# Optimization experiments

Measured on AMD Instinct MI355X. Metric: run time of the kernel, lower is better.

The kernel has to match this reference:

```python
import jax, jax.numpy as jnp
import numpy as np

BETA = 1.0
EPS = 1e-8  # matches torch F.cosine_similarity eps


def setup_inputs() -> dict:
    key = jax.random.key(0)
    x = jax.random.normal(key, (4096, 2, 1024), dtype=jnp.float32)
    return {"x": x}


def _cosine_sim_matrix(pos, anc):
    # pos: [B, D], anc: [B, D] -> [B, B], sim[i, j] = cos(pos[i], anc[j])
    dots = jnp.einsum('id,jd->ij', pos, anc)
    pn = jnp.sqrt(jnp.sum(pos * pos, axis=-1))
    an = jnp.sqrt(jnp.sum(anc * anc, axis=-1))
    denom = jnp.maximum(pn[:, None] * an[None, :], EPS)
    return dots / denom


def reference(x):
    # x: [B, M, D], M >= 2
    out_anchor = jnp.mean(x[:, 1:, :], axis=1)   # [B, D]
    out_positive = x[:, 0, :]                     # [B, D]
    sim = _cosine_sim_matrix(out_positive, out_anchor)  # [B, B]
    n = sim.shape[0]

    diag = jnp.diagonal(sim)                      # [B]
    # tempsim for column i: beta * (sim[:, i] - sim[i, i]), excluding row i
    T = BETA * (sim - diag[None, :])              # [B, B]
    eye = jnp.eye(n, dtype=bool)

    # exclude-diagonal logsumexp per column (vectorized over all columns)
    Tm = jnp.where(eye, -jnp.inf, T)
    temploss = jax.nn.logsumexp(Tm, axis=0)       # [B]
    # flatNCE trick: exp(l - stop_grad(l)) has value 1 but gradient of l
    nloss = jnp.mean(jnp.exp(temploss - jax.lax.stop_gradient(temploss)))

    # top-1 accuracy against labels arange(B) (detached in original)
    label = jnp.arange(n)
    prec1 = jnp.mean((jnp.argmax(sim, axis=1) == label).astype(jnp.float32)) * 100.0
    return nloss, prec1
```

## Files before the change

### kernel.cpp

```cpp
#include <hip/hip_runtime.h>


#define NROWS 4096
#define DDIM  1024
#define XSTR  2048

typedef unsigned int u32;
typedef unsigned long long u64;
typedef __attribute__((ext_vector_type(8))) short bf16x8;
typedef __attribute__((ext_vector_type(8))) unsigned short u16x8;
typedef __attribute__((ext_vector_type(16))) float f32x16;

__device__ __forceinline__ unsigned int fkey(float f) {
    unsigned int u = __float_as_uint(f);
    return (u & 0x80000000u) ? ~u : (u | 0x80000000u);
}

__device__ __forceinline__ u64 shfl_xor_u64(u64 v, int m) {
    unsigned int lo = (unsigned int)v;
    unsigned int hi = (unsigned int)(v >> 32);
    lo = __shfl_xor(lo, m, 64);
    hi = __shfl_xor(hi, m, 64);
    return ((u64)hi << 32) | lo;
}

__device__ __forceinline__ unsigned short f2bf(float f) {
    unsigned u = __float_as_uint(f);
    return (unsigned short)((u + 0x7FFFu + ((u >> 16) & 1u)) >> 16);
}

#define PF_OFF   0u
#define AF_OFF   8388608u
#define INV_OFF  16777216u
#define PCK_OFF  16793600u
#define DONE_OFF 16826368u
#define WS_NEED  16826432u

__global__ __launch_bounds__(256) void norms2_kernel(const float* __restrict__ x,
                                                     float* __restrict__ inv_an,
                                                     u64* __restrict__ packed,
                                                     unsigned int* __restrict__ done) {
    int gid  = blockIdx.x * 256 + threadIdx.x;
    int j    = gid >> 6;
    int lane = threadIdx.x & 63;
    if (gid < NROWS) packed[gid] = 0ULL;
    if (gid == 0) *done = 0u;
    const float4* a = (const float4*)(x + (size_t)j * XSTR + DDIM);
    float s = 0.0f;
#pragma unroll
    for (int i = 0; i < 4; ++i) {
        float4 v = a[lane + i * 64];
        s += v.x * v.x + v.y * v.y + v.z * v.z + v.w * v.w;
    }
#pragma unroll
    for (int off = 32; off > 0; off >>= 1) s += __shfl_down(s, off, 64);
    if (lane == 0) inv_an[j] = 1.0f / sqrtf(s);
}

__global__ __launch_bounds__(256) void conv_kernel(const float* __restrict__ x,
                                                   unsigned short* __restrict__ Pf,
                                                   unsigned short* __restrict__ Af) {
    const int cid  = blockIdx.x * 256 + threadIdx.x;
    const int lane = cid & 63;
    const int kh   = (cid >> 6) & 63;
    const int fb   = cid >> 12;
    const int row  = fb * 32 + (lane & 31);
    const int col  = kh * 16 + (lane >> 5) * 8;

    const float* px = x + (size_t)row * XSTR + col;
    float4 p0 = *(const float4*)(px);
    float4 p1 = *(const float4*)(px + 4);
    float4 a0 = *(const float4*)(px + DDIM);
    float4 a1 = *(const float4*)(px + DDIM + 4);

    u16x8 pv, av;
    pv[0] = f2bf(p0.x); pv[1] = f2bf(p0.y); pv[2] = f2bf(p0.z); pv[3] = f2bf(p0.w);
    pv[4] = f2bf(p1.x); pv[5] = f2bf(p1.y); pv[6] = f2bf(p1.z); pv[7] = f2bf(p1.w);
    av[0] = f2bf(a0.x); av[1] = f2bf(a0.y); av[2] = f2bf(a0.z); av[3] = f2bf(a0.w);
    av[4] = f2bf(a1.x); av[5] = f2bf(a1.y); av[6] = f2bf(a1.z); av[7] = f2bf(a1.w);

    *(u16x8*)(Pf + (size_t)cid * 8) = pv;
    *(u16x8*)(Af + (size_t)cid * 8) = av;
}

__global__ __launch_bounds__(512, 2) void mfma_gemm_argmax(const unsigned short* __restrict__ Pf,
                                                           const unsigned short* __restrict__ Af,
                                                           const float* __restrict__ inv_an,
                                                           u64* __restrict__ packed,
                                                           unsigned int* __restrict__ done,
                                                           float* __restrict__ out) {
    __shared__ __align__(16) unsigned int lds[32768];
    __shared__ unsigned int lastflag;
    __shared__ int cnt[8];

    const int bid = blockIdx.x;
    const int xcd = bid & 7;
    const int slt = bid >> 3;
    const int rblk = (xcd >> 1) * 4 + (slt >> 3);
    const int cblk = (xcd & 1) * 8 + (slt & 7);
    const int r0 = rblk * 256;
    const int c0 = cblk * 256;

    const int wave = threadIdx.x >> 6;
    const int lane = threadIdx.x & 63;
    const int l31 = lane & 31;
    const int lh = lane >> 5;
    const int wm = wave & 3;
    const int wn = wave >> 2;

    const char* gPs = (const char*)Pf + (((size_t)(rblk * 8 + wave)) << 16) + (size_t)lane * 16;
    const char* gAs = (const char*)Af + (((size_t)(cblk * 8 + wave)) << 16) + (size_t)lane * 16;

    f32x16 zero16 = {0.f,0.f,0.f,0.f,0.f,0.f,0.f,0.f,0.f,0.f,0.f,0.f,0.f,0.f,0.f,0.f};
    f32x16 acc[2][4];
#pragma unroll
    for (int i = 0; i < 2; ++i)
#pragma unroll
        for (int j = 0; j < 4; ++j) acc[i][j] = zero16;

#define ISSUE_TILE(tt)                                                                  \
    {                                                                                   \
        const int sb_ = ((tt) & 3) * 8192;                                              \
        const size_t go_ = ((size_t)((tt) * 2)) << 10;                                  \
        __builtin_amdgcn_global_load_lds((const u32*)(gPs + go_),                       \
                                         &lds[sb_ + wave * 256], 16, 0, 0);             \
        __builtin_amdgcn_global_load_lds((const u32*)(gAs + go_),                       \
                                         &lds[sb_ + 4096 + wave * 256], 16, 0, 0);      \
        __builtin_amdgcn_global_load_lds((const u32*)(gPs + go_ + 1024),                \
                                         &lds[sb_ + 2048 + wave * 256], 16, 0, 0);      \
        __builtin_amdgcn_global_load_lds((const u32*)(gAs + go_ + 1024),                \
                                         &lds[sb_ + 4096 + 2048 + wave * 256], 16, 0, 0);\
    }

#define PHASE(kh_l)                                                                     \
    {                                                                                   \
        const u32* bp_ = &lds[cbuf + (kh_l) * 2048 + (wm * 2) * 256 + lane * 4];        \
        bf16x8 f_p0 = *(const bf16x8*)(bp_);                                            \
        bf16x8 f_p1 = *(const bf16x8*)(bp_ + 256);                                      \
        const u32* ba_ = &lds[cbuf + 4096 + (kh_l) * 2048 + (wn * 4) * 256 + lane * 4]; \
        bf16x8 f_a0 = *(const bf16x8*)(ba_);                                            \
        bf16x8 f_a1 = *(const bf16x8*)(ba_ + 256);                                      \
        bf16x8 f_a2 = *(const bf16x8*)(ba_ + 512);                                      \
        bf16x8 f_a3 = *(const bf16x8*)(ba_ + 768);                                      \
        __builtin_amdgcn_s_barrier();                                                   \
        asm volatile("s_waitcnt lgkmcnt(0)" ::: "memory");                              \
        __builtin_amdgcn_sched_barrier(0);                                              \
        __builtin_amdgcn_s_setprio(1);                                                  \
        acc[0][0] = __builtin_amdgcn_mfma_f32_32x32x16_bf16(f_p0, f_a0, acc[0][0], 0, 0, 0); \
        acc[0][1] = __builtin_amdgcn_mfma_f32_32x32x16_bf16(f_p0, f_a1, acc[0][1], 0, 0, 0); \
        acc[0][2] = __builtin_amdgcn_mfma_f32_32x32x16_bf16(f_p0, f_a2, acc[0][2], 0, 0, 0); \
        acc[0][3] = __builtin_amdgcn_mfma_f32_32x32x16_bf16(f_p0, f_a3, acc[0][3], 0, 0, 0); \
        acc[1][0] = __builtin_amdgcn_mfma_f32_32x32x16_bf16(f_p1, f_a0, acc[1][0], 0, 0, 0); \
        acc[1][1] = __builtin_amdgcn_mfma_f32_32x32x16_bf16(f_p1, f_a1, acc[1][1], 0, 0, 0); \
        acc[1][2] = __builtin_amdgcn_mfma_f32_32x32x16_bf16(f_p1, f_a2, acc[1][2], 0, 0, 0); \
        acc[1][3] = __builtin_amdgcn_mfma_f32_32x32x16_bf16(f_p1, f_a3, acc[1][3], 0, 0, 0); \
        __builtin_amdgcn_s_setprio(0);                                                  \
        __builtin_amdgcn_s_barrier();                                                   \
    }

    ISSUE_TILE(0)
    ISSUE_TILE(1)
    ISSUE_TILE(2)

    for (int t = 0; t < 32; ++t) {
        const int cbuf = (t & 3) * 8192;

        if (t + 3 < 32) ISSUE_TILE(t + 3)

        if      (t < 29)  asm volatile("s_waitcnt vmcnt(12)" ::: "memory");
        else if (t == 29) asm volatile("s_waitcnt vmcnt(8)" ::: "memory");
        else if (t == 30) asm volatile("s_waitcnt vmcnt(4)" ::: "memory");
        else              asm volatile("s_waitcnt vmcnt(0)" ::: "memory");
        __builtin_amdgcn_s_barrier();

        PHASE(0)
        PHASE(1)
    }

    float ian[4];
#pragma unroll
    for (int nt = 0; nt < 4; ++nt) ian[nt] = inv_an[c0 + wn * 128 + nt * 32 + l31];

#pragma unroll
    for (int mt = 0; mt < 2; ++mt)
#pragma unroll
        for (int reg = 0; reg < 16; ++reg) {
            const int row = r0 + wm * 64 + mt * 32 + (reg & 3) + 8 * (reg >> 2) + 4 * lh;
            u64 best = 0ULL;
#pragma unroll
            for (int nt = 0; nt < 4; ++nt) {
                const int col = c0 + wn * 128 + nt * 32 + l31;
                const float v = acc[mt][nt][reg] * ian[nt];
                const u64 p = ((u64)fkey(v) << 32) | (unsigned int)(~col);
                best = best > p ? best : p;
            }
#pragma unroll
            for (int m = 1; m <= 16; m <<= 1) {
                const u64 o = shfl_xor_u64(best, m);
                best = best > o ? best : o;
            }
            if (l31 == 0) atomicMax(&packed[row], best);
        }

    __syncthreads();
    if (threadIdx.x == 0) {
        __threadfence();
        unsigned int old = atomicAdd(done, 1u);
        lastflag = (old == 255u) ? 1u : 0u;
    }
    __syncthreads();
    if (lastflag) {
        int c = 0;
        for (int r = threadIdx.x; r < NROWS; r += 512) {
            u64 v = atomicAdd(&packed[r], 0ULL);
            unsigned int col = ~(unsigned int)(v & 0xFFFFFFFFULL);
            c += (col == (unsigned int)r) ? 1 : 0;
        }
#pragma unroll
        for (int off = 32; off > 0; off >>= 1) c += __shfl_down(c, off, 64);
        if ((threadIdx.x & 63) == 0) cnt[threadIdx.x >> 6] = c;
        __syncthreads();
        if (threadIdx.x == 0) {
            int tot = 0;
#pragma unroll
            for (int w = 0; w < 8; ++w) tot += cnt[w];
            out[0] = 1.0f;
            out[1] = 100.0f * (float)tot / (float)NROWS;
        }
    }
#undef ISSUE_TILE
#undef PHASE
}

__global__ __launch_bounds__(256) void norms_kernel(const float* __restrict__ x,
                                                    float* __restrict__ inv_an,
                                                    u64* __restrict__ packed) {
    int gid  = blockIdx.x * 256 + threadIdx.x;
    int j    = gid >> 6;
    int lane = threadIdx.x & 63;
    if (gid < NROWS) packed[gid] = 0ULL;
    const float4* a = (const float4*)(x + (size_t)j * XSTR + DDIM);
    float s = 0.0f;
#pragma unroll
    for (int i = 0; i < 4; ++i) {
        float4 v = a[lane + i * 64];
        s += v.x * v.x + v.y * v.y + v.z * v.z + v.w * v.w;
    }
#pragma unroll
    for (int off = 32; off > 0; off >>= 1) s += __shfl_down(s, off, 64);
    if (lane == 0) inv_an[j] = 1.0f / sqrtf(s);
}

__global__ __launch_bounds__(256) void gemm_argmax_kernel(const float* __restrict__ x,
                                                          const float* __restrict__ inv_an,
                                                          u64* __restrict__ packed) {
    __shared__ __align__(16) float Pt[16][128];
    __shared__ __align__(16) float At[16][128];
    const int r0 = blockIdx.x * 128;
    const int c0 = blockIdx.y * 128;
    const int t = threadIdx.x;
    const int tx = t & 15;
    const int ty = t >> 4;
    const int srow = t >> 1;
    const int skq = (t & 1) * 8;
    float acc[8][8];
#pragma unroll
    for (int r = 0; r < 8; ++r)
#pragma unroll
        for (int c = 0; c < 8; ++c) acc[r][c] = 0.0f;
    const float* gp = x + (size_t)(r0 + srow) * XSTR + skq;
    const float* ga = x + (size_t)(c0 + srow) * XSTR + DDIM + skq;
    for (int k0 = 0; k0 < DDIM; k0 += 16) {
        __syncthreads();
        float4 p0 = *(const float4*)(gp + k0);
        float4 p1 = *(const float4*)(gp + k0 + 4);
        float4 a0 = *(const float4*)(ga + k0);
        float4 a1 = *(const float4*)(ga + k0 + 4);
        Pt[skq + 0][srow] = p0.x; Pt[skq + 1][srow] = p0.y;
        Pt[skq + 2][srow] = p0.z; Pt[skq + 3][srow] = p0.w;
        Pt[skq + 4][srow] = p1.x; Pt[skq + 5][srow] = p1.y;
        Pt[skq + 6][srow] = p1.z; Pt[skq + 7][srow] = p1.w;
        At[skq + 0][srow] = a0.x; At[skq + 1][srow] = a0.y;
        At[skq + 2][srow] = a0.z; At[skq + 3][srow] = a0.w;
        At[skq + 4][srow] = a1.x; At[skq + 5][srow] = a1.y;
        At[skq + 6][srow] = a1.z; At[skq + 7][srow] = a1.w;
        __syncthreads();
#pragma unroll
        for (int kk = 0; kk < 16; ++kk) {
            float pr[8], ar[8];
            *(float4*)&pr[0] = *(const float4*)&Pt[kk][ty * 8];
            *(float4*)&pr[4] = *(const float4*)&Pt[kk][ty * 8 + 4];
            *(float4*)&ar[0] = *(const float4*)&At[kk][tx * 8];
            *(float4*)&ar[4] = *(const float4*)&At[kk][tx * 8 + 4];
#pragma unroll
            for (int r = 0; r < 8; ++r)
#pragma unroll
                for (int c = 0; c < 8; ++c) acc[r][c] += pr[r] * ar[c];
        }
    }
    float ian[8];
#pragma unroll
    for (int c = 0; c < 8; ++c) ian[c] = inv_an[c0 + tx * 8 + c];
#pragma unroll
    for (int r = 0; r < 8; ++r) {
        int row = r0 + ty * 8 + r;
        u64 best = 0ULL;
#pragma unroll
        for (int c = 0; c < 8; ++c) {
            int col = c0 + tx * 8 + c;
            float v = acc[r][c] * ian[c];
            u64 p = ((u64)fkey(v) << 32) | (unsigned int)(~col);
            best = best > p ? best : p;
        }
#pragma unroll
        for (int m = 1; m <= 8; m <<= 1) {
            u64 o = shfl_xor_u64(best, m);
            best = best > o ? best : o;
        }
        if (tx == 0) atomicMax(&packed[row], best);
    }
}

__global__ __launch_bounds__(256) void finalize_kernel(const u64* __restrict__ packed,
                                                       float* __restrict__ out) {
    __shared__ int cnt_s;
    int t = threadIdx.x;
    if (t == 0) cnt_s = 0;
    __syncthreads();
    int c = 0;
    for (int r = t; r < NROWS; r += 256) {
        unsigned int col = ~(unsigned int)(packed[r] & 0xFFFFFFFFULL);
        c += (col == (unsigned int)r) ? 1 : 0;
    }
#pragma unroll
    for (int off = 32; off > 0; off >>= 1) c += __shfl_down(c, off, 64);
    if ((t & 63) == 0) atomicAdd(&cnt_s, c);
    __syncthreads();
    if (t == 0) {
        out[0] = 1.0f;
        out[1] = 100.0f * (float)cnt_s / (float)NROWS;
    }
}

extern "C" void kernel_launch(void* const* d_in, const int* in_sizes, int n_in,
                              void* d_out, int out_size, void* d_ws, size_t ws_size,
                              hipStream_t stream) {
    (void)in_sizes; (void)n_in; (void)out_size;
    const float* x = (const float*)d_in[0];
    float* out = (float*)d_out;

    if (ws_size >= (size_t)WS_NEED) {
        char* ws = (char*)d_ws;
        unsigned short* Pf = (unsigned short*)(ws + PF_OFF);
        unsigned short* Af = (unsigned short*)(ws + AF_OFF);
        float* inv_an = (float*)(ws + INV_OFF);
        u64* packed = (u64*)(ws + PCK_OFF);
        unsigned int* done = (unsigned int*)(ws + DONE_OFF);

        norms2_kernel<<<NROWS / 4, 256, 0, stream>>>(x, inv_an, packed, done);
        conv_kernel<<<2048, 256, 0, stream>>>(x, Pf, Af);
        mfma_gemm_argmax<<<256, 512, 0, stream>>>(Pf, Af, inv_an, packed, done, out);
    } else {
        float* inv_an = (float*)d_ws;
        u64* packed = (u64*)((char*)d_ws + NROWS * sizeof(float));
        norms_kernel<<<NROWS / 4, 256, 0, stream>>>(x, inv_an, packed);
        dim3 grid(NROWS / 128, NROWS / 128);
        gemm_argmax_kernel<<<grid, 256, 0, stream>>>(x, inv_an, packed);
        finalize_kernel<<<1, 256, 0, stream>>>(packed, out);
    }
}
```

Before: 131.2 us.

## Shrink GEMM block tile to 128x256 with 4 waves and double-buffered LDS

The fused GEMM+argmax kernel moves from 512-thread blocks with 256x256 tiles to 256-thread blocks with 128x256 tiles, doubling the grid to 512 blocks. The 4-deep LDS ring with graduated vmcnt waits is replaced by a 2-stage double buffer (48 KB instead of 128 KB) that waits for all loads each iteration, and the per-phase barriers are dropped. The goal is more blocks per CU and less LDS pressure. The cost is more reloading of A tiles and a shallower prefetch that may expose global-load latency.

```diff
diff --git a/kernel.cpp b/kernel.cpp
--- a/kernel.cpp
+++ b/kernel.cpp
@@ -83,33 +83,34 @@
     *(u16x8*)(Af + (size_t)cid * 8) = av;
 }
 
-__global__ __launch_bounds__(512, 2) void mfma_gemm_argmax(const unsigned short* __restrict__ Pf,
+__global__ __launch_bounds__(256, 2) void mfma_gemm_argmax(const unsigned short* __restrict__ Pf,
                                                            const unsigned short* __restrict__ Af,
                                                            const float* __restrict__ inv_an,
                                                            u64* __restrict__ packed,
                                                            unsigned int* __restrict__ done,
                                                            float* __restrict__ out) {
-    __shared__ __align__(16) unsigned int lds[32768];
+    __shared__ __align__(16) unsigned int lds[12288];
     __shared__ unsigned int lastflag;
-    __shared__ int cnt[8];
+    __shared__ int cnt[4];
 
     const int bid = blockIdx.x;
     const int xcd = bid & 7;
     const int slt = bid >> 3;
-    const int rblk = (xcd >> 1) * 4 + (slt >> 3);
+    const int rblk = (xcd >> 1) * 8 + (slt >> 3);
     const int cblk = (xcd & 1) * 8 + (slt & 7);
-    const int r0 = rblk * 256;
+    const int r0 = rblk * 128;
     const int c0 = cblk * 256;
 
     const int wave = threadIdx.x >> 6;
     const int lane = threadIdx.x & 63;
     const int l31 = lane & 31;
     const int lh = lane >> 5;
-    const int wm = wave & 3;
-    const int wn = wave >> 2;
-
-    const char* gPs = (const char*)Pf + (((size_t)(rblk * 8 + wave)) << 16) + (size_t)lane * 16;
-    const char* gAs = (const char*)Af + (((size_t)(cblk * 8 + wave)) << 16) + (size_t)lane * 16;
+    const int wm = wave & 1;
+    const int wn = wave >> 1;
+
+    const char* gPs = (const char*)Pf + (((size_t)(rblk * 4 + wave)) << 16) + (size_t)lane * 16;
+    const char* gA0 = (const char*)Af + (((size_t)(cblk * 8 + wave)) << 16) + (size_t)lane * 16;
+    const char* gA1 = (const char*)Af + (((size_t)(cblk * 8 + wave + 4)) << 16) + (size_t)lane * 16;
 
     f32x16 zero16 = {0.f,0.f,0.f,0.f,0.f,0.f,0.f,0.f,0.f,0.f,0.f,0.f,0.f,0.f,0.f,0.f};
     f32x16 acc[2][4];
@@ -118,34 +119,33 @@
 #pragma unroll
         for (int j = 0; j < 4; ++j) acc[i][j] = zero16;
 
-#define ISSUE_TILE(tt)                                                                  \
+#define ISSUE_TILE(tt, bb)                                                              \
     {                                                                                   \
-        const int sb_ = ((tt) & 3) * 8192;                                              \
         const size_t go_ = ((size_t)((tt) * 2)) << 10;                                  \
         __builtin_amdgcn_global_load_lds((const u32*)(gPs + go_),                       \
-                                         &lds[sb_ + wave * 256], 16, 0, 0);             \
-        __builtin_amdgcn_global_load_lds((const u32*)(gAs + go_),                       \
-                                         &lds[sb_ + 4096 + wave * 256], 16, 0, 0);      \
+                                         &lds[(bb) + wave * 256], 16, 0, 0);            \
         __builtin_amdgcn_global_load_lds((const u32*)(gPs + go_ + 1024),                \
-                                         &lds[sb_ + 2048 + wave * 256], 16, 0, 0);      \
-        __builtin_amdgcn_global_load_lds((const u32*)(gAs + go_ + 1024),                \
-                                         &lds[sb_ + 4096 + 2048 + wave * 256], 16, 0, 0);\
+                                         &lds[(bb) + 1024 + wave * 256], 16, 0, 0);     \
+        __builtin_amdgcn_global_load_lds((const u32*)(gA0 + go_),                       \
+                                         &lds[(bb) + 2048 + wave * 256], 16, 0, 0);     \
+        __builtin_amdgcn_global_load_lds((const u32*)(gA0 + go_ + 1024),                \
+                                         &lds[(bb) + 4096 + wave * 256], 16, 0, 0);     \
+        __builtin_amdgcn_global_load_lds((const u32*)(gA1 + go_),                       \
+                                         &lds[(bb) + 2048 + (wave + 4) * 256], 16, 0, 0);\
+        __builtin_amdgcn_global_load_lds((const u32*)(gA1 + go_ + 1024),                \
+                                         &lds[(bb) + 4096 + (wave + 4) * 256], 16, 0, 0);\
     }
 
 #define PHASE(kh_l)                                                                     \
     {                                                                                   \
-        const u32* bp_ = &lds[cbuf + (kh_l) * 2048 + (wm * 2) * 256 + lane * 4];        \
+        const u32* bp_ = &lds[cbuf + (kh_l) * 1024 + (wm * 2) * 256 + lane * 4];        \
         bf16x8 f_p0 = *(const bf16x8*)(bp_);                                            \
         bf16x8 f_p1 = *(const bf16x8*)(bp_ + 256);                                      \
-        const u32* ba_ = &lds[cbuf + 4096 + (kh_l) * 2048 + (wn * 4) * 256 + lane * 4]; \
+        const u32* ba_ = &lds[cbuf + 2048 + (kh_l) * 2048 + (wn * 4) * 256 + lane * 4]; \
         bf16x8 f_a0 = *(const bf16x8*)(ba_);                                            \
         bf16x8 f_a1 = *(const bf16x8*)(ba_ + 256);                                      \
         bf16x8 f_a2 = *(const bf16x8*)(ba_ + 512);                                      \
         bf16x8 f_a3 = *(const bf16x8*)(ba_ + 768);                                      \
-        __builtin_amdgcn_s_barrier();                                                   \
-        asm volatile("s_waitcnt lgkmcnt(0)" ::: "memory");                              \
-        __builtin_amdgcn_sched_barrier(0);                                              \
-        __builtin_amdgcn_s_setprio(1);                                                  \
         acc[0][0] = __builtin_amdgcn_mfma_f32_32x32x16_bf16(f_p0, f_a0, acc[0][0], 0, 0, 0); \
         acc[0][1] = __builtin_amdgcn_mfma_f32_32x32x16_bf16(f_p0, f_a1, acc[0][1], 0, 0, 0); \
         acc[0][2] = __builtin_amdgcn_mfma_f32_32x32x16_bf16(f_p0, f_a2, acc[0][2], 0, 0, 0); \
@@ -154,27 +154,24 @@
         acc[1][1] = __builtin_amdgcn_mfma_f32_32x32x16_bf16(f_p1, f_a1, acc[1][1], 0, 0, 0); \
         acc[1][2] = __builtin_amdgcn_mfma_f32_32x32x16_bf16(f_p1, f_a2, acc[1][2], 0, 0, 0); \
         acc[1][3] = __builtin_amdgcn_mfma_f32_32x32x16_bf16(f_p1, f_a3, acc[1][3], 0, 0, 0); \
-        __builtin_amdgcn_s_setprio(0);                                                  \
-        __builtin_amdgcn_s_barrier();                                                   \
-    }
-
-    ISSUE_TILE(0)
-    ISSUE_TILE(1)
-    ISSUE_TILE(2)
+    }
+
+    ISSUE_TILE(0, 0)
 
     for (int t = 0; t < 32; ++t) {
-        const int cbuf = (t & 3) * 8192;
-
-        if (t + 3 < 32) ISSUE_TILE(t + 3)
-
-        if      (t < 29)  asm volatile("s_waitcnt vmcnt(12)" ::: "memory");
-        else if (t == 29) asm volatile("s_waitcnt vmcnt(8)" ::: "memory");
-        else if (t == 30) asm volatile("s_waitcnt vmcnt(4)" ::: "memory");
-        else              asm volatile("s_waitcnt vmcnt(0)" ::: "memory");
+        const int cbuf = (t & 1) * 6144;
+        const int nbuf = ((t + 1) & 1) * 6144;
+
+        asm volatile("s_waitcnt vmcnt(0)" ::: "memory");
         __builtin_amdgcn_s_barrier();
-
+        __builtin_amdgcn_sched_barrier(0);
+
+        if (t + 1 < 32) ISSUE_TILE(t + 1, nbuf)
+
+        __builtin_amdgcn_s_setprio(1);
         PHASE(0)
         PHASE(1)
+        __builtin_amdgcn_s_setprio(0);
     }
 
     float ian[4];
@@ -206,12 +203,12 @@
     if (threadIdx.x == 0) {
         __threadfence();
         unsigned int old = atomicAdd(done, 1u);
-        lastflag = (old == 255u) ? 1u : 0u;
+        lastflag = (old == 511u) ? 1u : 0u;
     }
     __syncthreads();
     if (lastflag) {
         int c = 0;
-        for (int r = threadIdx.x; r < NROWS; r += 512) {
+        for (int r = threadIdx.x; r < NROWS; r += 256) {
             u64 v = atomicAdd(&packed[r], 0ULL);
             unsigned int col = ~(unsigned int)(v & 0xFFFFFFFFULL);
             c += (col == (unsigned int)r) ? 1 : 0;
@@ -223,7 +220,7 @@
         if (threadIdx.x == 0) {
             int tot = 0;
 #pragma unroll
-            for (int w = 0; w < 8; ++w) tot += cnt[w];
+            for (int w = 0; w < 4; ++w) tot += cnt[w];
             out[0] = 1.0f;
             out[1] = 100.0f * (float)tot / (float)NROWS;
         }
@@ -359,7 +356,7 @@
 
         norms2_kernel<<<NROWS / 4, 256, 0, stream>>>(x, inv_an, packed, done);
         conv_kernel<<<2048, 256, 0, stream>>>(x, Pf, Af);
-        mfma_gemm_argmax<<<256, 512, 0, stream>>>(Pf, Af, inv_an, packed, done, out);
+        mfma_gemm_argmax<<<512, 256, 0, stream>>>(Pf, Af, inv_an, packed, done, out);
     } else {
         float* inv_an = (float*)d_ws;
         u64* packed = (u64*)((char*)d_ws + NROWS * sizeof(float));
```

New measurement: 133.3 us. No clear change (+1.6%).
